# Kernel tuning notes

Measured on AMD Instinct MI355X. Metric: run time of the kernel, lower is better.

Reference implementation:

```python
import jax, jax.numpy as jnp
import numpy as np
import math

N_DRUG, N_DIS, D, EMB, HEADS, STEPS = 3072, 3072, 64, 16, 4, 5
N = N_DRUG + N_DIS


def setup_inputs() -> dict:
    key = jax.random.key(0)
    ks = jax.random.split(key, 16)
    s = lambda fan: 1.0 / np.sqrt(fan)
    return {
        "graph": jax.random.uniform(ks[0], (N, N), jnp.float32),
        "drug_f": jax.random.normal(ks[1], (N_DRUG, D), jnp.float32),
        "disease_f": jax.random.normal(ks[2], (N_DIS, D), jnp.float32),
        "timesteps": jax.random.randint(ks[3], (N,), 0, STEPS, jnp.int32),
        "drug_w": jax.random.normal(ks[4], (D, D), jnp.float32) * s(D),
        "disease_w": jax.random.normal(ks[5], (D, D), jnp.float32) * s(D),
        "emb_w": jax.random.normal(ks[6], (EMB, EMB), jnp.float32) * s(EMB),
        "emb_b": jnp.zeros((EMB,), jnp.float32),
        "in_w": jax.random.normal(ks[7], (D + EMB, 256), jnp.float32) * s(D + EMB),
        "in_b": jnp.zeros((256,), jnp.float32),
        "out_w": jax.random.normal(ks[8], (256, D), jnp.float32) * s(256),
        "out_b": jnp.zeros((D,), jnp.float32),
        "wq": jax.random.normal(ks[9], (D, D), jnp.float32) * s(D),
        "bq": jnp.zeros((D,), jnp.float32),
        "wk": jax.random.normal(ks[10], (D, D), jnp.float32) * s(D),
        "bk": jnp.zeros((D,), jnp.float32),
        "wv": jax.random.normal(ks[11], (D, D), jnp.float32) * s(D),
        "bv": jnp.zeros((D,), jnp.float32),
        "wo": jax.random.normal(ks[12], (D, D), jnp.float32) * s(D),
        "bo": jnp.zeros((D,), jnp.float32),
        "fuse_w": jax.random.normal(ks[13], (2 * D, D), jnp.float32) * s(2 * D),
        "fuse_b": jnp.zeros((D,), jnp.float32),
        "ln_g": jnp.ones((D,), jnp.float32),
        "ln_b": jnp.zeros((D,), jnp.float32),
    }


def _layernorm(x, g, b, eps=1e-5):
    mu = jnp.mean(x, axis=-1, keepdims=True)
    var = jnp.var(x, axis=-1, keepdims=True)
    return (x - mu) * jax.lax.rsqrt(var + eps) * g + b


def reference(graph, drug_f, disease_f, timesteps, drug_w, disease_w,
              emb_w, emb_b, in_w, in_b, out_w, out_b,
              wq, bq, wk, bk, wv, bv, wo, bo,
              fuse_w, fuse_b, ln_g, ln_b):
    # ---- DGLLayer: per-type projection + symmetric degree-norm propagation ----
    node_f = jnp.concatenate([drug_f @ drug_w, disease_f @ disease_w], axis=0)  # [N, D]
    degs = jnp.clip(jnp.sum(graph, axis=1), 1.0, None)
    norm = jax.lax.rsqrt(degs)[:, None]  # degs^-0.5, [N, 1]
    target = (graph @ (node_f * norm)) * norm

    # ---- Denoise MLP with sinusoidal time embedding ----
    half = EMB // 2
    freqs = jnp.exp(-math.log(10000.0) * jnp.arange(half, dtype=jnp.float32) / half)
    temp = timesteps.astype(jnp.float32)[:, None] * freqs[None]  # [N, half]
    time_emb = jnp.concatenate([jnp.cos(temp), jnp.sin(temp)], axis=-1)  # [N, EMB]
    emb = time_emb @ emb_w + emb_b
    h = jnp.concatenate([target, emb], axis=-1)  # [N, D+EMB]
    h = jnp.tanh(h @ in_w + in_b)  # in-layer
    aux = h @ out_w + out_b        # final out-layer (no tanh)

    # ---- AttentionFusion: cross-attention(target -> aux) + fuse + residual LN ----
    hd = D // HEADS
    q = (target @ wq + bq).reshape(N, HEADS, hd)
    k = (aux @ wk + bk).reshape(N, HEADS, hd)
    v = (aux @ wv + bv).reshape(N, HEADS, hd)
    scores = jnp.einsum('nhd,mhd->hnm', q, k) / np.sqrt(hd)  # [H, N, N]
    attn = jax.nn.softmax(scores, axis=-1)
    attn_out = jnp.einsum('hnm,mhd->nhd', attn, v).reshape(N, D) @ wo + bo
    fused = jnp.concatenate([target, attn_out], axis=-1) @ fuse_w + fuse_b
    return _layernorm(fused + target, ln_g, ln_b)
```

## Files before the change

kernel.cpp:

```cpp
#include <hip/hip_runtime.h>
#include <cstdint>
#include <cstddef>

#define NTOT 6144
#define NDRUG 3072
#define NM (NTOT*64)

typedef __fp16 f16;
typedef __attribute__((ext_vector_type(2))) __fp16 f16x2;
typedef __attribute__((ext_vector_type(4))) __fp16 f16x4;
typedef __attribute__((ext_vector_type(8))) __fp16 f16x8;
typedef __attribute__((ext_vector_type(4))) float f32x4;

__device__ __forceinline__ f16x8 pack8(float4 a, float4 b){
  f16x2 p0 = __builtin_amdgcn_cvt_pkrtz(a.x, a.y);
  f16x2 p1 = __builtin_amdgcn_cvt_pkrtz(a.z, a.w);
  f16x2 p2 = __builtin_amdgcn_cvt_pkrtz(b.x, b.y);
  f16x2 p3 = __builtin_amdgcn_cvt_pkrtz(b.z, b.w);
  f16x4 lo = __builtin_shufflevector(p0, p1, 0, 1, 2, 3);
  f16x4 hi = __builtin_shufflevector(p2, p3, 0, 1, 2, 3);
  return __builtin_shufflevector(lo, hi, 0, 1, 2, 3, 4, 5, 6, 7);
}

__global__ __launch_bounds__(256) void k_rowsum(const float* __restrict__ g,
                                                float* __restrict__ norm){
  int wv = threadIdx.x >> 6, lane = threadIdx.x & 63;
  int row = blockIdx.x*4 + wv;
  const float4* p = (const float4*)(g + (size_t)row * NTOT);
  float s = 0.f;
  #pragma unroll
  for (int it = 0; it < 24; ++it) {
    float4 u = p[it*64 + lane];
    s += u.x + u.y + u.z + u.w;
  }
  #pragma unroll
  for (int off = 32; off; off >>= 1) s += __shfl_xor(s, off, 64);
  if (lane == 0) norm[row] = rsqrtf(fmaxf(s, 1.0f));
}

__global__ __launch_bounds__(256) void k_nodef(const float* __restrict__ drug_f,
                                               const float* __restrict__ dis_f,
                                               const float* __restrict__ drug_w,
                                               const float* __restrict__ dis_w,
                                               const float* __restrict__ norm,
                                               float* __restrict__ nfs){
  __shared__ float sx[4][64];
  int wv = threadIdx.x>>6, j = threadIdx.x&63;
  int row = blockIdx.x*4 + wv;
  const float* x; const float* W;
  if (row < NDRUG){ x = drug_f + (size_t)row*64; W = drug_w; }
  else            { x = dis_f + (size_t)(row-NDRUG)*64; W = dis_w; }
  sx[wv][j] = x[j];
  __syncthreads();
  float acc = 0.f;
  #pragma unroll 8
  for (int k = 0; k < 64; ++k) acc = fmaf(sx[wv][k], W[k*64+j], acc);
  nfs[(size_t)row*64 + j] = acc * norm[row];
}

__global__ __launch_bounds__(256) void k_gemm(const float* __restrict__ graph,
                                              const float* __restrict__ nfs,
                                              float* __restrict__ part){
  __shared__ f16 sA[64][72];
  __shared__ f16 sBt[64][72];
  const int tid = threadIdx.x;
  const int lane = tid & 63, w = tid >> 6;
  const int l15 = lane & 15, quad = lane >> 4;
  const int row0 = blockIdx.x * 64;
  const int kbase = blockIdx.y * 768;

  f32x4 acc[4] = {{0.f,0.f,0.f,0.f},{0.f,0.f,0.f,0.f},
                  {0.f,0.f,0.f,0.f},{0.f,0.f,0.f,0.f}};

  const int ar = tid >> 2, acg = (tid & 3) * 16;
  const int bk = (tid & 31) * 2, bng = (tid >> 5) * 8;

  for (int kt = 0; kt < 12; ++kt){
    const int k0 = kbase + kt*64;
    __syncthreads();
    {
      const float4* srcA = (const float4*)(graph + (size_t)(row0 + ar)*NTOT + k0 + acg);
      float4 a0 = srcA[0], a1 = srcA[1], a2 = srcA[2], a3 = srcA[3];
      *(f16x8*)&sA[ar][acg]     = pack8(a0, a1);
      *(f16x8*)&sA[ar][acg + 8] = pack8(a2, a3);
      const float4* b0p = (const float4*)(nfs + (size_t)(k0 + bk)*64 + bng);
      const float4* b1p = (const float4*)(nfs + (size_t)(k0 + bk + 1)*64 + bng);
      float4 r00 = b0p[0], r01 = b0p[1];
      float4 r10 = b1p[0], r11 = b1p[1];
      float e0[8] = {r00.x,r00.y,r00.z,r00.w,r01.x,r01.y,r01.z,r01.w};
      float e1[8] = {r10.x,r10.y,r10.z,r10.w,r11.x,r11.y,r11.z,r11.w};
      #pragma unroll
      for (int i = 0; i < 8; ++i){
        f16x2 pr = __builtin_amdgcn_cvt_pkrtz(e0[i], e1[i]);
        *(f16x2*)&sBt[bng + i][bk] = pr;
      }
    }
    __syncthreads();
    #pragma unroll
    for (int k16 = 0; k16 < 4; ++k16){
      f16x4 af = *(const f16x4*)&sA[w*16 + l15][k16*16 + quad*4];
      #pragma unroll
      for (int nt = 0; nt < 4; ++nt){
        f16x4 bf = *(const f16x4*)&sBt[nt*16 + l15][k16*16 + quad*4];
        acc[nt] = __builtin_amdgcn_mfma_f32_16x16x16f16(af, bf, acc[nt], 0, 0, 0);
      }
    }
  }
  float* dst = part + (size_t)blockIdx.y * NM;
  #pragma unroll
  for (int nt = 0; nt < 4; ++nt){
    #pragma unroll
    for (int r = 0; r < 4; ++r){
      int row = row0 + w*16 + quad*4 + r;
      dst[(size_t)row*64 + nt*16 + l15] = acc[nt][r];
    }
  }
}

__global__ __launch_bounds__(256) void k_finish(const float* __restrict__ part,
                                                const float* __restrict__ norm,
                                                float* __restrict__ target){
  size_t idx = (size_t)blockIdx.x*256 + threadIdx.x;
  int row = (int)(idx >> 6);
  float s = 0.f;
  #pragma unroll
  for (int p = 0; p < 8; ++p) s += part[(size_t)p*NM + idx];
  target[idx] = s * norm[row];
}

__global__ __launch_bounds__(256) void k_mlp(const int* __restrict__ ts,
                                             const float* __restrict__ target,
                                             const float* __restrict__ emb_w,
                                             const float* __restrict__ emb_b,
                                             const float* __restrict__ in_w,
                                             const float* __restrict__ in_b,
                                             const float* __restrict__ out_w,
                                             const float* __restrict__ out_b,
                                             float* __restrict__ aux){
  __shared__ float sx[4][80];
  __shared__ float sh[4][256];
  int wv = threadIdx.x>>6, j = threadIdx.x&63;
  int row = blockIdx.x*4 + wv;
  sx[wv][j] = target[(size_t)row*64 + j];
  if (j < 16) {
    const float FREQ[8] = {1.0f, 0.316227766016838f, 0.1f, 0.0316227766016838f,
                           0.01f, 0.00316227766016838f, 0.001f, 0.000316227766016838f};
    float t = (float)ts[row];
    float e = emb_b[j];
    #pragma unroll
    for (int k = 0; k < 8; ++k) {
      float a = t * FREQ[k];
      e = fmaf(cosf(a), emb_w[k*16 + j], e);
      e = fmaf(sinf(a), emb_w[(8+k)*16 + j], e);
    }
    sx[wv][64 + j] = e;
  }
  __syncthreads();
  float a0 = in_b[4*j+0], a1 = in_b[4*j+1], a2 = in_b[4*j+2], a3 = in_b[4*j+3];
  #pragma unroll 8
  for (int k = 0; k < 80; ++k) {
    float xv = sx[wv][k];
    float4 w = *(const float4*)(in_w + k*256 + 4*j);
    a0 = fmaf(xv, w.x, a0);
    a1 = fmaf(xv, w.y, a1);
    a2 = fmaf(xv, w.z, a2);
    a3 = fmaf(xv, w.w, a3);
  }
  sh[wv][4*j+0] = tanhf(a0); sh[wv][4*j+1] = tanhf(a1);
  sh[wv][4*j+2] = tanhf(a2); sh[wv][4*j+3] = tanhf(a3);
  __syncthreads();
  float o = out_b[j];
  #pragma unroll 8
  for (int k = 0; k < 256; ++k) o = fmaf(sh[wv][k], out_w[k*64 + j], o);
  aux[(size_t)row*64 + j] = o;
}

__global__ __launch_bounds__(256) void k_qkv(const float* __restrict__ target,
                                             const float* __restrict__ aux,
                                             const float* __restrict__ wq, const float* __restrict__ bq,
                                             const float* __restrict__ wk, const float* __restrict__ bk,
                                             const float* __restrict__ wvw, const float* __restrict__ bv,
                                             float* __restrict__ qb, float* __restrict__ kb,
                                             float* __restrict__ vb){
  __shared__ float st[4][64], sa[4][64];
  int wv = threadIdx.x>>6, j = threadIdx.x&63;
  int row = blockIdx.x*4 + wv;
  st[wv][j] = target[(size_t)row*64+j];
  sa[wv][j] = aux[(size_t)row*64+j];
  __syncthreads();
  float q = bq[j], kk = bk[j], vv = bv[j];
  #pragma unroll 8
  for (int k = 0; k < 64; ++k) {
    float t = st[wv][k], a = sa[wv][k];
    q  = fmaf(t, wq[k*64+j],  q);
    kk = fmaf(a, wk[k*64+j],  kk);
    vv = fmaf(a, wvw[k*64+j], vv);
  }
  qb[(size_t)row*64+j]=q; kb[(size_t)row*64+j]=kk; vb[(size_t)row*64+j]=vv;
}

__global__ __launch_bounds__(256) void k_attn(const float* __restrict__ qb,
                                              const float* __restrict__ kb,
                                              const float* __restrict__ vb,
                                              float* __restrict__ pattn){
  __shared__ f16 sK[64][72];
  __shared__ f16 sV[64][72];
  const int tid = threadIdx.x;
  const int h = tid >> 6;
  const int lane = tid & 63;
  const int l15 = lane & 15, quad = lane >> 4;
  const int z = blockIdx.y;
  const int q0 = blockIdx.x * 64;

  f16x4 qf[4];
  #pragma unroll
  for (int qn = 0; qn < 4; ++qn){
    float4 v = *(const float4*)(qb + (size_t)(q0 + qn*16 + l15)*64 + h*16 + quad*4);
    f16x2 lo = __builtin_amdgcn_cvt_pkrtz(v.x, v.y);
    f16x2 hi = __builtin_amdgcn_cvt_pkrtz(v.z, v.w);
    qf[qn] = __builtin_shufflevector(lo, hi, 0, 1, 2, 3);
  }

  f32x4 accOT[4] = {{0.f,0.f,0.f,0.f},{0.f,0.f,0.f,0.f},
                    {0.f,0.f,0.f,0.f},{0.f,0.f,0.f,0.f}};
  float lsum[4] = {0.f, 0.f, 0.f, 0.f};

  const int kbase = z * 768;
  for (int kt = 0; kt < 12; ++kt){
    const int k0 = kbase + kt*64;
    __syncthreads();
    {
      const int key = tid >> 2, dc = (tid & 3) * 16;
      const float4* srcK = (const float4*)(kb + (size_t)(k0 + key)*64 + dc);
      const float4* srcV = (const float4*)(vb + (size_t)(k0 + key)*64 + dc);
      float4 ka = srcK[0], kbv = srcK[1], kc = srcK[2], kd = srcK[3];
      float4 va = srcV[0], vbv = srcV[1], vc = srcV[2], vd = srcV[3];
      *(f16x8*)&sK[key][dc]     = pack8(ka, kbv);
      *(f16x8*)&sK[key][dc + 8] = pack8(kc, kd);
      *(f16x8*)&sV[key][dc]     = pack8(va, vbv);
      *(f16x8*)&sV[key][dc + 8] = pack8(vc, vd);
    }
    __syncthreads();
    #pragma unroll
    for (int km = 0; km < 4; ++km){
      f16x4 kf = *(const f16x4*)&sK[km*16 + l15][h*16 + quad*4];
      f16x4 vf;
      vf[0] = sV[km*16 + quad*4 + 0][h*16 + l15];
      vf[1] = sV[km*16 + quad*4 + 1][h*16 + l15];
      vf[2] = sV[km*16 + quad*4 + 2][h*16 + l15];
      vf[3] = sV[km*16 + quad*4 + 3][h*16 + l15];
      #pragma unroll
      for (int qn = 0; qn < 4; ++qn){
        f32x4 s = __builtin_amdgcn_mfma_f32_16x16x16f16(
            kf, qf[qn], (f32x4){0.f,0.f,0.f,0.f}, 0, 0, 0);
        float p0 = __expf(fminf(s[0]*0.25f, 10.f));
        float p1 = __expf(fminf(s[1]*0.25f, 10.f));
        float p2 = __expf(fminf(s[2]*0.25f, 10.f));
        float p3 = __expf(fminf(s[3]*0.25f, 10.f));
        lsum[qn] += (p0 + p1) + (p2 + p3);
        f16x2 plo = __builtin_amdgcn_cvt_pkrtz(p0, p1);
        f16x2 phi = __builtin_amdgcn_cvt_pkrtz(p2, p3);
        f16x4 pf = __builtin_shufflevector(plo, phi, 0, 1, 2, 3);
        accOT[qn] = __builtin_amdgcn_mfma_f32_16x16x16f16(vf, pf, accOT[qn], 0, 0, 0);
      }
    }
  }
  #pragma unroll
  for (int qn = 0; qn < 4; ++qn){
    lsum[qn] += __shfl_xor(lsum[qn], 16, 64);
    lsum[qn] += __shfl_xor(lsum[qn], 32, 64);
  }
  #pragma unroll
  for (int qn = 0; qn < 4; ++qn){
    float* rec = pattn + ((size_t)(z*4 + h)*NTOT + q0 + qn*16 + l15) * 20;
    *(float4*)(rec + quad*4) =
        make_float4(accOT[qn][0], accOT[qn][1], accOT[qn][2], accOT[qn][3]);
    if (quad == 0){ rec[16] = 0.f; rec[17] = lsum[qn]; }
  }
}

__global__ __launch_bounds__(256) void k_attn_fin(const float* __restrict__ pattn,
                                                  float* __restrict__ attnb){
  int idx = blockIdx.x*256 + threadIdx.x;
  int h = idx / NTOT;
  int row = idx % NTOT;
  float M = -1e30f;
  #pragma unroll
  for (int z = 0; z < 8; ++z)
    M = fmaxf(M, pattn[((size_t)(z*4 + h)*NTOT + row)*20 + 16]);
  float L = 0.f;
  float o[16];
  #pragma unroll
  for (int d = 0; d < 16; ++d) o[d] = 0.f;
  #pragma unroll
  for (int z = 0; z < 8; ++z) {
    const float* rec = pattn + ((size_t)(z*4 + h)*NTOT + row)*20;
    float e = __expf(rec[16] - M);
    L = fmaf(rec[17], e, L);
    #pragma unroll
    for (int d = 0; d < 16; ++d) o[d] = fmaf(rec[d], e, o[d]);
  }
  float inv = 1.0f / L;
  #pragma unroll
  for (int d = 0; d < 16; ++d)
    attnb[(size_t)row*64 + h*16 + d] = o[d] * inv;
}

__global__ __launch_bounds__(256) void k_fuse(const float* __restrict__ target,
                                              const float* __restrict__ attnb,
                                              const float* __restrict__ wo, const float* __restrict__ bo,
                                              const float* __restrict__ fuse_w, const float* __restrict__ fuse_b,
                                              const float* __restrict__ ln_g, const float* __restrict__ ln_b,
                                              float* __restrict__ out){
  __shared__ float st[4][64], sa[4][64], sao[4][64];
  int wv = threadIdx.x>>6, j = threadIdx.x&63;
  int row = blockIdx.x*4 + wv;
  st[wv][j] = target[(size_t)row*64+j];
  sa[wv][j] = attnb[(size_t)row*64+j];
  __syncthreads();
  float ao = bo[j];
  #pragma unroll 8
  for (int k = 0; k < 64; ++k) ao = fmaf(sa[wv][k], wo[k*64+j], ao);
  sao[wv][j] = ao;
  __syncthreads();
  float f = fuse_b[j];
  #pragma unroll 8
  for (int k = 0; k < 64; ++k) f = fmaf(st[wv][k], fuse_w[k*64+j], f);
  #pragma unroll 8
  for (int k = 0; k < 64; ++k) f = fmaf(sao[wv][k], fuse_w[(64+k)*64+j], f);
  float x = f + st[wv][j];
  float s1 = x, s2 = x*x;
  #pragma unroll
  for (int off = 32; off; off >>= 1) { s1 += __shfl_xor(s1, off, 64); s2 += __shfl_xor(s2, off, 64); }
  float mu = s1*(1.f/64.f);
  float var = s2*(1.f/64.f) - mu*mu;
  float y = (x-mu)*rsqrtf(var + 1e-5f)*ln_g[j] + ln_b[j];
  out[(size_t)row*64 + j] = y;
}

extern "C" void kernel_launch(void* const* d_in, const int* in_sizes, int n_in,
                              void* d_out, int out_size, void* d_ws, size_t ws_size,
                              hipStream_t stream) {
  const float* graph  = (const float*)d_in[0];
  const float* drug_f = (const float*)d_in[1];
  const float* dis_f  = (const float*)d_in[2];
  const int*   ts     = (const int*)d_in[3];
  const float* drug_w = (const float*)d_in[4];
  const float* dis_w  = (const float*)d_in[5];
  const float* emb_w  = (const float*)d_in[6];
  const float* emb_b  = (const float*)d_in[7];
  const float* in_w   = (const float*)d_in[8];
  const float* in_b   = (const float*)d_in[9];
  const float* out_w  = (const float*)d_in[10];
  const float* out_b  = (const float*)d_in[11];
  const float* wq     = (const float*)d_in[12];
  const float* bq     = (const float*)d_in[13];
  const float* wk     = (const float*)d_in[14];
  const float* bk     = (const float*)d_in[15];
  const float* wvw    = (const float*)d_in[16];
  const float* bv     = (const float*)d_in[17];
  const float* wo     = (const float*)d_in[18];
  const float* bo     = (const float*)d_in[19];
  const float* fuse_w = (const float*)d_in[20];
  const float* fuse_b = (const float*)d_in[21];
  const float* ln_g   = (const float*)d_in[22];
  const float* ln_b   = (const float*)d_in[23];

  float* ws     = (float*)d_ws;
  float* norm   = ws;
  float* nfs    = norm + 8192;
  float* target = nfs + NM;
  float* aux    = target + NM;
  float* qb     = aux + NM;
  float* kb     = qb + NM;
  float* vb     = kb + NM;
  float* attnb  = vb + NM;
  float* part   = attnb + NM;
  float* pattn  = part + (size_t)8*NM;

  k_rowsum<<<1536, 256, 0, stream>>>(graph, norm);
  k_nodef<<<1536, 256, 0, stream>>>(drug_f, dis_f, drug_w, dis_w, norm, nfs);
  k_gemm<<<dim3(96, 8), 256, 0, stream>>>(graph, nfs, part);
  k_finish<<<1536, 256, 0, stream>>>(part, norm, target);
  k_mlp<<<1536, 256, 0, stream>>>(ts, target, emb_w, emb_b, in_w, in_b, out_w, out_b, aux);
  k_qkv<<<1536, 256, 0, stream>>>(target, aux, wq, bq, wk, bk, wvw, bv, qb, kb, vb);
  k_attn<<<dim3(96, 8), 256, 0, stream>>>(qb, kb, vb, pattn);
  k_attn_fin<<<96, 256, 0, stream>>>(pattn, attnb);
  k_fuse<<<1536, 256, 0, stream>>>(target, attnb, wo, bo, fuse_w, fuse_b, ln_g, ln_b, (float*)d_out);
}
```

Before: 413.5 us.

## Fuse node-wise kernels and attention finish, transpose V in shared memory

Merges the degree row-sum with the node projection, the partial-sum finish with the MLP and QKV projections, and the attention combine with the output fusion/LayerNorm, cutting launches and intermediate global buffers (aux, attnb). V is stored transposed in LDS so MFMA B-fragments load as one vector read. The attention combine drops max rescaling since partial max was always zero, relying on that invariant.

Result: faster. 404.0 us (-2.3%).

```diff
diff --git a/kernel.cpp b/kernel.cpp
--- a/kernel.cpp
+++ b/kernel.cpp
@@ -22,31 +22,28 @@
   return __builtin_shufflevector(lo, hi, 0, 1, 2, 3, 4, 5, 6, 7);
 }
 
-__global__ __launch_bounds__(256) void k_rowsum(const float* __restrict__ g,
-                                                float* __restrict__ norm){
-  int wv = threadIdx.x >> 6, lane = threadIdx.x & 63;
+__global__ __launch_bounds__(256) void k_deg(const float* __restrict__ g,
+                                             const float* __restrict__ drug_f,
+                                             const float* __restrict__ dis_f,
+                                             const float* __restrict__ drug_w,
+                                             const float* __restrict__ dis_w,
+                                             float* __restrict__ norm,
+                                             float* __restrict__ nfs){
+  __shared__ float sx[4][64];
+  int wv = threadIdx.x >> 6, j = threadIdx.x & 63;
   int row = blockIdx.x*4 + wv;
   const float4* p = (const float4*)(g + (size_t)row * NTOT);
   float s = 0.f;
   #pragma unroll
   for (int it = 0; it < 24; ++it) {
-    float4 u = p[it*64 + lane];
+    float4 u = p[it*64 + j];
     s += u.x + u.y + u.z + u.w;
   }
   #pragma unroll
   for (int off = 32; off; off >>= 1) s += __shfl_xor(s, off, 64);
-  if (lane == 0) norm[row] = rsqrtf(fmaxf(s, 1.0f));
-}
-
-__global__ __launch_bounds__(256) void k_nodef(const float* __restrict__ drug_f,
-                                               const float* __restrict__ dis_f,
-                                               const float* __restrict__ drug_w,
-                                               const float* __restrict__ dis_w,
-                                               const float* __restrict__ norm,
-                                               float* __restrict__ nfs){
-  __shared__ float sx[4][64];
-  int wv = threadIdx.x>>6, j = threadIdx.x&63;
-  int row = blockIdx.x*4 + wv;
+  float nrm = rsqrtf(fmaxf(s, 1.0f));
+  if (j == 0) norm[row] = nrm;
+
   const float* x; const float* W;
   if (row < NDRUG){ x = drug_f + (size_t)row*64; W = drug_w; }
   else            { x = dis_f + (size_t)(row-NDRUG)*64; W = dis_w; }
@@ -55,7 +52,7 @@
   float acc = 0.f;
   #pragma unroll 8
   for (int k = 0; k < 64; ++k) acc = fmaf(sx[wv][k], W[k*64+j], acc);
-  nfs[(size_t)row*64 + j] = acc * norm[row];
+  nfs[(size_t)row*64 + j] = acc * nrm;
 }
 
 __global__ __launch_bounds__(256) void k_gemm(const float* __restrict__ graph,
@@ -117,39 +114,41 @@
   }
 }
 
-__global__ __launch_bounds__(256) void k_finish(const float* __restrict__ part,
-                                                const float* __restrict__ norm,
-                                                float* __restrict__ target){
-  size_t idx = (size_t)blockIdx.x*256 + threadIdx.x;
-  int row = (int)(idx >> 6);
-  float s = 0.f;
-  #pragma unroll
-  for (int p = 0; p < 8; ++p) s += part[(size_t)p*NM + idx];
-  target[idx] = s * norm[row];
-}
-
-__global__ __launch_bounds__(256) void k_mlp(const int* __restrict__ ts,
-                                             const float* __restrict__ target,
-                                             const float* __restrict__ emb_w,
-                                             const float* __restrict__ emb_b,
-                                             const float* __restrict__ in_w,
-                                             const float* __restrict__ in_b,
-                                             const float* __restrict__ out_w,
-                                             const float* __restrict__ out_b,
-                                             float* __restrict__ aux){
+__global__ __launch_bounds__(256) void k_node2(const float* __restrict__ part,
+                                               const float* __restrict__ norm,
+                                               const int* __restrict__ ts,
+                                               const float* __restrict__ emb_w,
+                                               const float* __restrict__ emb_b,
+                                               const float* __restrict__ in_w,
+                                               const float* __restrict__ in_b,
+                                               const float* __restrict__ out_w,
+                                               const float* __restrict__ out_b,
+                                               const float* __restrict__ wq, const float* __restrict__ bq,
+                                               const float* __restrict__ wk, const float* __restrict__ bk,
+                                               const float* __restrict__ wvw, const float* __restrict__ bv,
+                                               float* __restrict__ target,
+                                               float* __restrict__ qb, float* __restrict__ kb,
+                                               float* __restrict__ vb){
   __shared__ float sx[4][80];
   __shared__ float sh[4][256];
+  __shared__ float sa[4][64];
   int wv = threadIdx.x>>6, j = threadIdx.x&63;
   int row = blockIdx.x*4 + wv;
-  sx[wv][j] = target[(size_t)row*64 + j];
+
+  float t = 0.f;
+  #pragma unroll
+  for (int p = 0; p < 8; ++p) t += part[(size_t)p*NM + (size_t)row*64 + j];
+  t *= norm[row];
+  target[(size_t)row*64 + j] = t;
+  sx[wv][j] = t;
   if (j < 16) {
     const float FREQ[8] = {1.0f, 0.316227766016838f, 0.1f, 0.0316227766016838f,
                            0.01f, 0.00316227766016838f, 0.001f, 0.000316227766016838f};
-    float t = (float)ts[row];
+    float tt = (float)ts[row];
     float e = emb_b[j];
     #pragma unroll
     for (int k = 0; k < 8; ++k) {
-      float a = t * FREQ[k];
+      float a = tt * FREQ[k];
       e = fmaf(cosf(a), emb_w[k*16 + j], e);
       e = fmaf(sinf(a), emb_w[(8+k)*16 + j], e);
     }
@@ -172,29 +171,15 @@
   float o = out_b[j];
   #pragma unroll 8
   for (int k = 0; k < 256; ++k) o = fmaf(sh[wv][k], out_w[k*64 + j], o);
-  aux[(size_t)row*64 + j] = o;
-}
-
-__global__ __launch_bounds__(256) void k_qkv(const float* __restrict__ target,
-                                             const float* __restrict__ aux,
-                                             const float* __restrict__ wq, const float* __restrict__ bq,
-                                             const float* __restrict__ wk, const float* __restrict__ bk,
-                                             const float* __restrict__ wvw, const float* __restrict__ bv,
-                                             float* __restrict__ qb, float* __restrict__ kb,
-                                             float* __restrict__ vb){
-  __shared__ float st[4][64], sa[4][64];
-  int wv = threadIdx.x>>6, j = threadIdx.x&63;
-  int row = blockIdx.x*4 + wv;
-  st[wv][j] = target[(size_t)row*64+j];
-  sa[wv][j] = aux[(size_t)row*64+j];
+  sa[wv][j] = o;
   __syncthreads();
   float q = bq[j], kk = bk[j], vv = bv[j];
   #pragma unroll 8
   for (int k = 0; k < 64; ++k) {
-    float t = st[wv][k], a = sa[wv][k];
-    q  = fmaf(t, wq[k*64+j],  q);
-    kk = fmaf(a, wk[k*64+j],  kk);
-    vv = fmaf(a, wvw[k*64+j], vv);
+    float tv = sx[wv][k], av = sa[wv][k];
+    q  = fmaf(tv, wq[k*64+j],  q);
+    kk = fmaf(av, wk[k*64+j],  kk);
+    vv = fmaf(av, wvw[k*64+j], vv);
   }
   qb[(size_t)row*64+j]=q; kb[(size_t)row*64+j]=kk; vb[(size_t)row*64+j]=vv;
 }
@@ -204,7 +189,7 @@
                                               const float* __restrict__ vb,
                                               float* __restrict__ pattn){
   __shared__ f16 sK[64][72];
-  __shared__ f16 sV[64][72];
+  __shared__ f16 sVt[64][72];
   const int tid = threadIdx.x;
   const int h = tid >> 6;
   const int lane = tid & 63;
@@ -225,30 +210,35 @@
                     {0.f,0.f,0.f,0.f},{0.f,0.f,0.f,0.f}};
   float lsum[4] = {0.f, 0.f, 0.f, 0.f};
 
+  const int kr = tid >> 2, kdc = (tid & 3) * 16;
+  const int vk = (tid & 31) * 2, vdg = (tid >> 5) * 8;
+
   const int kbase = z * 768;
   for (int kt = 0; kt < 12; ++kt){
     const int k0 = kbase + kt*64;
     __syncthreads();
     {
-      const int key = tid >> 2, dc = (tid & 3) * 16;
-      const float4* srcK = (const float4*)(kb + (size_t)(k0 + key)*64 + dc);
-      const float4* srcV = (const float4*)(vb + (size_t)(k0 + key)*64 + dc);
+      const float4* srcK = (const float4*)(kb + (size_t)(k0 + kr)*64 + kdc);
       float4 ka = srcK[0], kbv = srcK[1], kc = srcK[2], kd = srcK[3];
-      float4 va = srcV[0], vbv = srcV[1], vc = srcV[2], vd = srcV[3];
-      *(f16x8*)&sK[key][dc]     = pack8(ka, kbv);
-      *(f16x8*)&sK[key][dc + 8] = pack8(kc, kd);
-      *(f16x8*)&sV[key][dc]     = pack8(va, vbv);
-      *(f16x8*)&sV[key][dc + 8] = pack8(vc, vd);
+      *(f16x8*)&sK[kr][kdc]     = pack8(ka, kbv);
+      *(f16x8*)&sK[kr][kdc + 8] = pack8(kc, kd);
+      const float4* v0p = (const float4*)(vb + (size_t)(k0 + vk)*64 + vdg);
+      const float4* v1p = (const float4*)(vb + (size_t)(k0 + vk + 1)*64 + vdg);
+      float4 r00 = v0p[0], r01 = v0p[1];
+      float4 r10 = v1p[0], r11 = v1p[1];
+      float e0[8] = {r00.x,r00.y,r00.z,r00.w,r01.x,r01.y,r01.z,r01.w};
+      float e1[8] = {r10.x,r10.y,r10.z,r10.w,r11.x,r11.y,r11.z,r11.w};
+      #pragma unroll
+      for (int i = 0; i < 8; ++i){
+        f16x2 pr = __builtin_amdgcn_cvt_pkrtz(e0[i], e1[i]);
+        *(f16x2*)&sVt[vdg + i][vk] = pr;
+      }
     }
     __syncthreads();
     #pragma unroll
     for (int km = 0; km < 4; ++km){
       f16x4 kf = *(const f16x4*)&sK[km*16 + l15][h*16 + quad*4];
-      f16x4 vf;
-      vf[0] = sV[km*16 + quad*4 + 0][h*16 + l15];
-      vf[1] = sV[km*16 + quad*4 + 1][h*16 + l15];
-      vf[2] = sV[km*16 + quad*4 + 2][h*16 + l15];
-      vf[3] = sV[km*16 + quad*4 + 3][h*16 + l15];
+      f16x4 vf = *(const f16x4*)&sVt[h*16 + l15][km*16 + quad*4];
       #pragma unroll
       for (int qn = 0; qn < 4; ++qn){
         f32x4 s = __builtin_amdgcn_mfma_f32_16x16x16f16(
@@ -275,48 +265,29 @@
     float* rec = pattn + ((size_t)(z*4 + h)*NTOT + q0 + qn*16 + l15) * 20;
     *(float4*)(rec + quad*4) =
         make_float4(accOT[qn][0], accOT[qn][1], accOT[qn][2], accOT[qn][3]);
-    if (quad == 0){ rec[16] = 0.f; rec[17] = lsum[qn]; }
-  }
-}
-
-__global__ __launch_bounds__(256) void k_attn_fin(const float* __restrict__ pattn,
-                                                  float* __restrict__ attnb){
-  int idx = blockIdx.x*256 + threadIdx.x;
-  int h = idx / NTOT;
-  int row = idx % NTOT;
-  float M = -1e30f;
-  #pragma unroll
-  for (int z = 0; z < 8; ++z)
-    M = fmaxf(M, pattn[((size_t)(z*4 + h)*NTOT + row)*20 + 16]);
-  float L = 0.f;
-  float o[16];
-  #pragma unroll
-  for (int d = 0; d < 16; ++d) o[d] = 0.f;
-  #pragma unroll
-  for (int z = 0; z < 8; ++z) {
-    const float* rec = pattn + ((size_t)(z*4 + h)*NTOT + row)*20;
-    float e = __expf(rec[16] - M);
-    L = fmaf(rec[17], e, L);
-    #pragma unroll
-    for (int d = 0; d < 16; ++d) o[d] = fmaf(rec[d], e, o[d]);
-  }
-  float inv = 1.0f / L;
-  #pragma unroll
-  for (int d = 0; d < 16; ++d)
-    attnb[(size_t)row*64 + h*16 + d] = o[d] * inv;
-}
-
-__global__ __launch_bounds__(256) void k_fuse(const float* __restrict__ target,
-                                              const float* __restrict__ attnb,
-                                              const float* __restrict__ wo, const float* __restrict__ bo,
-                                              const float* __restrict__ fuse_w, const float* __restrict__ fuse_b,
-                                              const float* __restrict__ ln_g, const float* __restrict__ ln_b,
-                                              float* __restrict__ out){
+    if (quad == 0){ rec[17] = lsum[qn]; }
+  }
+}
+
+__global__ __launch_bounds__(256) void k_out(const float* __restrict__ pattn,
+                                             const float* __restrict__ target,
+                                             const float* __restrict__ wo, const float* __restrict__ bo,
+                                             const float* __restrict__ fuse_w, const float* __restrict__ fuse_b,
+                                             const float* __restrict__ ln_g, const float* __restrict__ ln_b,
+                                             float* __restrict__ out){
   __shared__ float st[4][64], sa[4][64], sao[4][64];
   int wv = threadIdx.x>>6, j = threadIdx.x&63;
   int row = blockIdx.x*4 + wv;
+  int h = j >> 4, d = j & 15;
+  float osum = 0.f, L = 0.f;
+  #pragma unroll
+  for (int z = 0; z < 8; ++z) {
+    const float* rec = pattn + ((size_t)(z*4 + h)*NTOT + row)*20;
+    osum += rec[d];
+    L += rec[17];
+  }
+  sa[wv][j] = osum / L;
   st[wv][j] = target[(size_t)row*64+j];
-  sa[wv][j] = attnb[(size_t)row*64+j];
   __syncthreads();
   float ao = bo[j];
   #pragma unroll 8
@@ -370,21 +341,18 @@
   float* norm   = ws;
   float* nfs    = norm + 8192;
   float* target = nfs + NM;
-  float* aux    = target + NM;
-  float* qb     = aux + NM;
+  float* qb     = target + NM;
   float* kb     = qb + NM;
   float* vb     = kb + NM;
-  float* attnb  = vb + NM;
-  float* part   = attnb + NM;
+  float* part   = vb + NM;
   float* pattn  = part + (size_t)8*NM;
 
-  k_rowsum<<<1536, 256, 0, stream>>>(graph, norm);
-  k_nodef<<<1536, 256, 0, stream>>>(drug_f, dis_f, drug_w, dis_w, norm, nfs);
+  k_deg<<<1536, 256, 0, stream>>>(graph, drug_f, dis_f, drug_w, dis_w, norm, nfs);
   k_gemm<<<dim3(96, 8), 256, 0, stream>>>(graph, nfs, part);
-  k_finish<<<1536, 256, 0, stream>>>(part, norm, target);
-  k_mlp<<<1536, 256, 0, stream>>>(ts, target, emb_w, emb_b, in_w, in_b, out_w, out_b, aux);
-  k_qkv<<<1536, 256, 0, stream>>>(target, aux, wq, bq, wk, bk, wvw, bv, qb, kb, vb);
+  k_node2<<<1536, 256, 0, stream>>>(part, norm, ts, emb_w, emb_b, in_w, in_b,
+                                    out_w, out_b, wq, bq, wk, bk, wvw, bv,
+                                    target, qb, kb, vb);
   k_attn<<<dim3(96, 8), 256, 0, stream>>>(qb, kb, vb, pattn);
-  k_attn_fin<<<96, 256, 0, stream>>>(pattn, attnb);
-  k_fuse<<<1536, 256, 0, stream>>>(target, attnb, wo, bo, fuse_w, fuse_b, ln_g, ln_b, (float*)d_out);
-}
+  k_out<<<1536, 256, 0, stream>>>(pattn, target, wo, bo, fuse_w, fuse_b,
+                                  ln_g, ln_b, (float*)d_out);
+}
```
